# Performance work log

Measured on AMD Instinct MI355X. Metric: run time of the kernel, lower is better.

The kernel has to match this reference:

```python
import jax, jax.numpy as jnp
import numpy as np

HEADS = 8
DIM = 64
L = 2
P = 4  # hard-coded p_num in the torch module


def conv2d(x, w, b=None, pad=0, groups=1):
    y = jax.lax.conv_general_dilated(x, w, (1, 1), [(pad, pad), (pad, pad)],
        dimension_numbers=('NCHW', 'OIHW', 'NCHW'), feature_group_count=groups)
    return y if b is None else y + b[None, :, None, None]


def conv3d(x, w, pad=1, groups=1):
    return jax.lax.conv_general_dilated(x, w, (1, 1, 1), [(pad, pad)] * 3,
        dimension_numbers=('NCDHW', 'OIDHW', 'NCDHW'), feature_group_count=groups)


def pw(x, w):  # 1x1 conv, w: [O, C]
    return jnp.einsum('oc,bchw->bohw', w, x)


def layernorm(x, w, b):  # WithBias_LayerNorm over channel dim of NCHW
    mu = x.mean(axis=1, keepdims=True)
    var = ((x - mu) ** 2).mean(axis=1, keepdims=True)
    return (x - mu) / jnp.sqrt(var + 1e-5) * w[None, :, None, None] + b[None, :, None, None]


def l2n(x):  # F.normalize(dim=-1, p=2)
    return x / jnp.maximum(jnp.linalg.norm(x, axis=-1, keepdims=True), 1e-12)


def gelu(x):
    return jax.nn.gelu(x, approximate=False)


def spec_attn(x, mask, wq, wk, wv, dwq, dwk, dwv, resc, wp, mp1, mp2):
    b, c, h, w = x.shape
    ch = c // HEADS
    q = conv2d(pw(x, wq), dwq, pad=1, groups=c).reshape(b, HEADS, ch, h * w)
    k = conv2d(pw(x, wk), dwk, pad=1, groups=c).reshape(b, HEADS, ch, h * w)
    v = conv2d(pw(x, wv), dwv, pad=1, groups=c).reshape(b, HEADS, ch, h * w)
    q, k = l2n(q), l2n(k)
    att = jnp.einsum('bhcn,bhdn->bhcd', q, k) * resc[None, :, None, None]
    mb = pw(jax.nn.relu(conv2d(mask, mp1, pad=1)), mp2).mean(axis=(2, 3)).reshape(b, HEADS, ch)
    att = att + mb[:, :, None, :] - mb[:, :, :, None]
    att = jax.nn.softmax(att, axis=-1)
    out = jnp.einsum('bhcd,bhdn->bhcn', att, v).reshape(b, c, h, w)
    return pw(out, wp)


def ffn2d(x, w1, w2):  # PreNorm: dwconv3x3 (groups=dim, out=4*dim) -> GELU -> 1x1
    return pw(gelu(conv2d(x, w1, pad=1, groups=DIM)), w2)


def pol_attn(x, mask, wq, wk, wv, pwt, pb, resc, m1w, m1b, m2w, m2b):
    bp, c, h, w = x.shape
    bn = bp // P
    ch = c // HEADS
    xt = x.reshape(bn, P, c, h, w).transpose(0, 3, 4, 1, 2).reshape(bn * h * w, P, c)
    def heads_(t):
        return t.reshape(-1, P, HEADS, ch).transpose(0, 2, 1, 3)
    q = l2n(heads_(xt @ wq.T))
    k = l2n(heads_(xt @ wk.T))
    v = heads_(xt @ wv.T)
    att = jnp.einsum('bhpc,bhqc->bhpq', q, k) * resc[None, :, None, None]
    mg = pw(gelu(conv2d(mask, m1w, m1b, pad=1, groups=c)), m2w) + m2b[None, :, None, None]
    mg = mg.reshape(bn, P, c, h, w).mean(axis=2).transpose(0, 2, 3, 1).reshape(bn * h * w, P)
    att = att + (mg[:, None, :] - mg[:, :, None])[:, None]
    att = jax.nn.softmax(att, axis=-1)
    o = jnp.einsum('bhpq,bhqc->bhpc', att, v).transpose(0, 2, 1, 3).reshape(-1, P, c)
    o = o @ pwt.T + pb
    return o.reshape(bn, h, w, P, c).transpose(0, 3, 4, 1, 2).reshape(bp, c, h, w)


def ffn3d(x, w1, w2):  # PreNorm_Pols: 3D dwconv over (p,h,w) -> GELU -> 1x1x1
    bp, c, h, w = x.shape
    bn = bp // P
    y = x.reshape(bn, P, c, h, w).transpose(0, 2, 1, 3, 4)  # [bn, c, p, h, w]
    y = gelu(conv3d(y, w1, pad=1, groups=DIM))
    y = jnp.einsum('oc,bcdhw->bodhw', w2, y)
    return y.transpose(0, 2, 1, 3, 4).reshape(bp, c, h, w)


def forward(x, mask, sl1w, sl1b, sl2w, sl2b, swq, swk, swv, sdq, sdk, sdv, sresc, sproj,
            smp1, smp2, sf1, sf2, pl1w, pl1b, pl2w, pl2b, pwq, pwk, pwv, ppw, ppb, presc,
            pm1w, pm1b, pm2w, pm2b, pf1, pf2, fw1, fb1, fw2, fb2):
    # PSAM with type='pols': spectral branch + cross-polar branch + sigmoid fusion
    xs = x
    for i in range(L):
        xs = spec_attn(layernorm(xs, sl1w[i], sl1b[i]), mask, swq[i], swk[i], swv[i],
                       sdq[i], sdk[i], sdv[i], sresc[i], sproj[i], smp1[i], smp2[i]) + xs
        xs = ffn2d(layernorm(xs, sl2w[i], sl2b[i]), sf1[i], sf2[i]) + xs
    xp = x
    for i in range(L):
        xp = pol_attn(layernorm(xp, pl1w[i], pl1b[i]), mask, pwq[i], pwk[i], pwv[i],
                      ppw[i], ppb[i], presc[i], pm1w[i], pm1b[i], pm2w[i], pm2b[i]) + xp
        xp = ffn3d(layernorm(xp, pl2w[i], pl2b[i]), pf1[i], pf2[i]) + xp
    fu = jnp.concatenate([xs, xp], axis=1)
    a = jax.nn.sigmoid(conv2d(jax.nn.relu(pw(fu, fw1) + fb1[None, :, None, None]), fw2, fb2, pad=1))
    return a * xs + (1 - a) * xp


def setup_inputs():
    key = jax.random.key(0)
    D, H, Lb, B = DIM, HEADS, L, 8
    cnt = [0]
    def nrm(shape, s=0.02):
        cnt[0] += 1
        return jax.random.normal(jax.random.fold_in(key, cnt[0]), shape, jnp.float32) * s
    d = {}
    d['x'] = jax.random.normal(jax.random.fold_in(key, 1000), (B, D, 128, 128), jnp.float32)
    d['mask'] = jax.random.uniform(jax.random.fold_in(key, 1001), (B, D, 128, 128), jnp.float32)
    d['sl1w'] = jnp.ones((Lb, D)); d['sl1b'] = jnp.zeros((Lb, D))
    d['sl2w'] = jnp.ones((Lb, D)); d['sl2b'] = jnp.zeros((Lb, D))
    for n in ['swq', 'swk', 'swv', 'sproj', 'smp2']:
        d[n] = nrm((Lb, D, D))
    for n in ['sdq', 'sdk', 'sdv']:
        d[n] = nrm((Lb, D, 1, 3, 3))
    d['smp1'] = nrm((Lb, D, D, 3, 3))
    d['sresc'] = jnp.ones((Lb, H))
    d['sf1'] = nrm((Lb, 4 * D, 1, 3, 3)); d['sf2'] = nrm((Lb, D, 4 * D))
    d['pl1w'] = jnp.ones((Lb, D)); d['pl1b'] = jnp.zeros((Lb, D))
    d['pl2w'] = jnp.ones((Lb, D)); d['pl2b'] = jnp.zeros((Lb, D))
    for n in ['pwq', 'pwk', 'pwv', 'ppw', 'pm2w']:
        d[n] = nrm((Lb, D, D))
    d['ppb'] = jnp.zeros((Lb, D)); d['presc'] = jnp.ones((Lb, H))
    d['pm1w'] = nrm((Lb, D, 1, 3, 3)); d['pm1b'] = jnp.zeros((Lb, D)); d['pm2b'] = jnp.zeros((Lb, D))
    d['pf1'] = nrm((Lb, 4 * D, 1, 3, 3, 3)); d['pf2'] = nrm((Lb, D, 4 * D))
    d['fw1'] = nrm((D, 2 * D)); d['fb1'] = jnp.zeros((D,))
    d['fw2'] = nrm((D, D, 3, 3)); d['fb2'] = jnp.zeros((D,))
    return d


def reference(x, mask, sl1w, sl1b, sl2w, sl2b, swq, swk, swv, sdq, sdk, sdv, sresc, sproj,
              smp1, smp2, sf1, sf2, pl1w, pl1b, pl2w, pl2b, pwq, pwk, pwv, ppw, ppb, presc,
              pm1w, pm1b, pm2w, pm2b, pf1, pf2, fw1, fb1, fw2, fb2):
    return forward(x, mask, sl1w, sl1b, sl2w, sl2b, swq, swk, swv, sdq, sdk, sdv, sresc, sproj,
                   smp1, smp2, sf1, sf2, pl1w, pl1b, pl2w, pl2b, pwq, pwk, pwv, ppw, ppb, presc,
                   pm1w, pm1b, pm2w, pm2b, pf1, pf2, fw1, fb1, fw2, fb2)
```

## Files before the change

kernel.cpp:

```cpp
#include <hip/hip_runtime.h>
#include <math.h>

#define NPIX 16384
#define SBUF 8388608

__device__ __forceinline__ float gelu_f(float x){
    return 0.5f*x*(1.0f+erff(x*0.70710678118654752440f));
}
__device__ __forceinline__ float waveReduceSum(float v){
    #pragma unroll
    for(int off=32;off>0;off>>=1) v += __shfl_down(v, off);
    return v;
}

__global__ __launch_bounds__(256) void ln_kernel(const float* __restrict__ x,
        const float* __restrict__ w, const float* __restrict__ b, float* __restrict__ out){
    int idx = blockIdx.x*256 + threadIdx.x;
    int bb = idx >> 14, n = idx & 16383;
    const float* ip = x + ((size_t)bb<<20) + n;
    float v[64]; float s = 0.f;
    #pragma unroll
    for(int c=0;c<64;c++){ v[c] = ip[(size_t)c<<14]; s += v[c]; }
    float mu = s*(1.f/64.f); float ss = 0.f;
    #pragma unroll
    for(int c=0;c<64;c++){ float d = v[c]-mu; ss += d*d; }
    float r = rsqrtf(ss*(1.f/64.f) + 1e-5f);
    float* op = out + ((size_t)bb<<20) + n;
    #pragma unroll
    for(int c=0;c<64;c++) op[(size_t)c<<14] = (v[c]-mu)*r*w[c] + b[c];
}

__global__ __launch_bounds__(256) void pw_kernel(const float* __restrict__ in,
        const float* __restrict__ w, const float* __restrict__ bias,
        const float* __restrict__ res, float* __restrict__ out, int wPerB){
    __shared__ float wl[4096];
    int t = threadIdx.x;
    int idx = blockIdx.x*256 + t;
    int b = idx >> 14, n = idx & 16383;
    const float* wp = w + (wPerB ? b*4096 : 0);
    for(int i=t;i<4096;i+=256) wl[(i&63)*64 + (i>>6)] = wp[i];
    __syncthreads();
    float acc[64];
    if(bias){
        #pragma unroll
        for(int o=0;o<64;o++) acc[o] = bias[o];
    } else {
        #pragma unroll
        for(int o=0;o<64;o++) acc[o] = 0.f;
    }
    const float* ip = in + ((size_t)b<<20) + n;
    for(int c=0;c<64;c++){
        float v = ip[(size_t)c<<14];
        const float4* wv = (const float4*)&wl[c*64];
        #pragma unroll
        for(int o4=0;o4<16;o4++){
            float4 w4 = wv[o4];
            acc[o4*4+0] += w4.x*v; acc[o4*4+1] += w4.y*v;
            acc[o4*4+2] += w4.z*v; acc[o4*4+3] += w4.w*v;
        }
    }
    size_t baseo = ((size_t)b<<20) + n;
    if(res){
        #pragma unroll
        for(int o=0;o<64;o++) out[baseo+((size_t)o<<14)] = acc[o] + res[baseo+((size_t)o<<14)];
    } else {
        #pragma unroll
        for(int o=0;o<64;o++) out[baseo+((size_t)o<<14)] = acc[o];
    }
}

__global__ __launch_bounds__(256) void dw3x3_kernel(const float* __restrict__ in,
        const float* __restrict__ wd, float* __restrict__ out){
    int idx = blockIdx.x*256 + threadIdx.x;
    int n = idx & 16383; int bc = idx >> 14; int c = bc & 63;
    int y = n >> 7, x = n & 127;
    bool ym=y>0, yp=y<127, xm=x>0, xpv=x<127;
    const float* cp = in + ((size_t)bc<<14) + n;
    const float* wp = wd + c*9;
    float s = cp[0]*wp[4];
    if(ym){ s += cp[-128]*wp[1]; if(xm) s += cp[-129]*wp[0]; if(xpv) s += cp[-127]*wp[2]; }
    if(xm)  s += cp[-1]*wp[3];
    if(xpv) s += cp[1]*wp[5];
    if(yp){ s += cp[128]*wp[7]; if(xm) s += cp[127]*wp[6]; if(xpv) s += cp[129]*wp[8]; }
    out[idx] = s;
}

__global__ __launch_bounds__(256) void l2n_kernel(float* __restrict__ q){
    int bc = blockIdx.x;
    float* p = q + ((size_t)bc<<14);
    int t = threadIdx.x;
    float ss = 0.f;
    for(int n=t;n<NPIX;n+=256){ float v=p[n]; ss += v*v; }
    ss = waveReduceSum(ss);
    __shared__ float red[4];
    __shared__ float scale_s;
    if((t&63)==0) red[t>>6] = ss;
    __syncthreads();
    if(t==0) scale_s = 1.f/fmaxf(sqrtf(red[0]+red[1]+red[2]+red[3]), 1e-12f);
    __syncthreads();
    float sc = scale_s;
    for(int n=t;n<NPIX;n+=256) p[n] *= sc;
}

__global__ __launch_bounds__(256) void qk_kernel(const float* __restrict__ Q,
        const float* __restrict__ K, float* __restrict__ att){
    int blk = blockIdx.x;
    int c = blk & 7, bh = blk >> 3;
    const float* qp = Q + (((size_t)bh*8 + c)<<14);
    const float* kp = K + (((size_t)bh*8)<<14);
    float p[8] = {0,0,0,0,0,0,0,0};
    for(int n=threadIdx.x;n<NPIX;n+=256){
        float qv = qp[n];
        #pragma unroll
        for(int d=0;d<8;d++) p[d] += qv*kp[((size_t)d<<14)+n];
    }
    #pragma unroll
    for(int off=32;off>0;off>>=1){
        #pragma unroll
        for(int d=0;d<8;d++) p[d] += __shfl_down(p[d], off);
    }
    __shared__ float red[4][8];
    int wave = threadIdx.x>>6, lane = threadIdx.x&63;
    if(lane==0){
        #pragma unroll
        for(int d=0;d<8;d++) red[wave][d] = p[d];
    }
    __syncthreads();
    if(threadIdx.x<8){
        float s = red[0][threadIdx.x]+red[1][threadIdx.x]+red[2][threadIdx.x]+red[3][threadIdx.x];
        att[blk*8+threadIdx.x] = s;
    }
}

__global__ void zero512(float* __restrict__ p){
    p[blockIdx.x*256 + threadIdx.x] = 0.f;
}

__global__ __launch_bounds__(256) void mbconv4_kernel(const float* __restrict__ mask,
        const float* __restrict__ w, float* __restrict__ svec){
    __shared__ float wl[9216];
    __shared__ float red[4][16];
    int t = threadIdx.x;
    int og = blockIdx.x & 3;
    int pb = (blockIdx.x >> 2) & 31;
    int b  = blockIdx.x >> 7;
    const float* wp = w + (size_t)og*16*576;
    for(int i=t;i<9216;i+=256){
        int mo = i & 15, ck = i >> 4;
        wl[i] = wp[mo*576 + ck];
    }
    __syncthreads();
    int n0 = pb*512 + t;
    int n1 = n0 + 256;
    int y0 = n0>>7, x0 = n0&127;
    int y1 = n1>>7, x1 = n1&127;
    bool ym0=y0>0, yp0=y0<127, xm0=x0>0, xp0=x0<127;
    bool ym1=y1>0, yp1=y1<127, xm1=x1>0, xp1=x1<127;
    const float* mp = mask + ((size_t)b<<20);
    float acc0[16], acc1[16];
    #pragma unroll
    for(int o=0;o<16;o++){ acc0[o]=0.f; acc1[o]=0.f; }
    for(int c=0;c<64;c++){
        const float* cp0 = mp + ((size_t)c<<14) + n0;
        const float* cp1 = mp + ((size_t)c<<14) + n1;
        float ta[9], tb[9];
        ta[0] = (ym0&&xm0)? cp0[-129]:0.f;
        ta[1] =  ym0?       cp0[-128]:0.f;
        ta[2] = (ym0&&xp0)? cp0[-127]:0.f;
        ta[3] =  xm0?       cp0[-1]:0.f;
        ta[4] =             cp0[0];
        ta[5] =  xp0?       cp0[1]:0.f;
        ta[6] = (yp0&&xm0)? cp0[127]:0.f;
        ta[7] =  yp0?       cp0[128]:0.f;
        ta[8] = (yp0&&xp0)? cp0[129]:0.f;
        tb[0] = (ym1&&xm1)? cp1[-129]:0.f;
        tb[1] =  ym1?       cp1[-128]:0.f;
        tb[2] = (ym1&&xp1)? cp1[-127]:0.f;
        tb[3] =  xm1?       cp1[-1]:0.f;
        tb[4] =             cp1[0];
        tb[5] =  xp1?       cp1[1]:0.f;
        tb[6] = (yp1&&xm1)? cp1[127]:0.f;
        tb[7] =  yp1?       cp1[128]:0.f;
        tb[8] = (yp1&&xp1)? cp1[129]:0.f;
        #pragma unroll
        for(int k=0;k<9;k++){
            float va = ta[k], vb = tb[k];
            const float4* wv = (const float4*)&wl[(c*9+k)*16];
            #pragma unroll
            for(int o4=0;o4<4;o4++){
                float4 w4 = wv[o4];
                acc0[o4*4+0] += w4.x*va; acc0[o4*4+1] += w4.y*va;
                acc0[o4*4+2] += w4.z*va; acc0[o4*4+3] += w4.w*va;
                acc1[o4*4+0] += w4.x*vb; acc1[o4*4+1] += w4.y*vb;
                acc1[o4*4+2] += w4.z*vb; acc1[o4*4+3] += w4.w*vb;
            }
        }
    }
    int wave = t>>6, lane = t&63;
    #pragma unroll
    for(int m=0;m<16;m++){
        float v = waveReduceSum(fmaxf(acc0[m],0.f) + fmaxf(acc1[m],0.f));
        if(lane==0) red[wave][m] = v;
    }
    __syncthreads();
    if(t<16){
        float s = red[0][t]+red[1][t]+red[2][t]+red[3][t];
        atomicAdd(&svec[b*64 + og*16 + t], s);
    }
}

__global__ void spec_softmax_kernel(float* __restrict__ att, const float* __restrict__ svec,
        const float* __restrict__ smp2, const float* __restrict__ resc){
    int b = blockIdx.x, t = threadIdx.x;
    __shared__ float mb[64];
    float a = 0.f;
    for(int m=0;m<64;m++) a += smp2[t*64+m]*svec[b*64+m];
    mb[t] = a*(1.f/16384.f);
    __syncthreads();
    int h = t>>3, c = t&7;
    float* ap = att + (size_t)(b*8+h)*64 + c*8;
    float rs = resc[h];
    float v[8]; float mx = -1e30f;
    #pragma unroll
    for(int d=0;d<8;d++){ v[d] = ap[d]*rs + mb[h*8+d] - mb[h*8+c]; mx = fmaxf(mx, v[d]); }
    float s = 0.f;
    #pragma unroll
    for(int d=0;d<8;d++){ v[d] = expf(v[d]-mx); s += v[d]; }
    float inv = 1.f/s;
    #pragma unroll
    for(int d=0;d<8;d++) ap[d] = v[d]*inv;
}

__global__ void mmat_kernel(const float* __restrict__ att, const float* __restrict__ sproj,
        float* __restrict__ M){
    int b = blockIdx.x;
    for(int e=threadIdx.x;e<4096;e+=256){
        int o = e>>6, j = e&63;
        int h = j>>3, jj = j&7;
        float s = 0.f;
        #pragma unroll
        for(int cc=0;cc<8;cc++) s += sproj[o*64 + h*8+cc]*att[(size_t)(b*8+h)*64 + cc*8 + jj];
        M[b*4096 + e] = s;
    }
}

__global__ __launch_bounds__(256) void ffn2d_kernel(const float* __restrict__ A,
        const float* __restrict__ w1, const float* __restrict__ w2, float* __restrict__ xs){
    __shared__ float w2l[16384];
    int t = threadIdx.x;
    for(int i=t;i<16384;i+=256){ int o=i>>8, m=i&255; w2l[m*64+o] = w2[i]; }
    __syncthreads();
    int idx = blockIdx.x*256 + t;
    int b = idx>>14, n = idx&16383;
    int y = n>>7, x = n&127;
    bool ym=y>0, yp=y<127, xm=x>0, xpv=x<127;
    const float* ap = A + ((size_t)b<<20) + n;
    float acc[64];
    #pragma unroll
    for(int o=0;o<64;o++) acc[o] = 0.f;
    for(int c=0;c<64;c++){
        const float* cp = ap + ((size_t)c<<14);
        float t00 = (ym&&xm)? cp[-129]:0.f;
        float t01 =  ym?      cp[-128]:0.f;
        float t02 = (ym&&xpv)?cp[-127]:0.f;
        float t10 =  xm?      cp[-1]:0.f;
        float t11 =           cp[0];
        float t12 =  xpv?     cp[1]:0.f;
        float t20 = (yp&&xm)? cp[127]:0.f;
        float t21 =  yp?      cp[128]:0.f;
        float t22 = (yp&&xpv)?cp[129]:0.f;
        const float* w1c = w1 + c*36;
        #pragma unroll
        for(int j=0;j<4;j++){
            const float* wj = w1c + j*9;
            float cv = t00*wj[0]+t01*wj[1]+t02*wj[2]+t10*wj[3]+t11*wj[4]
                      +t12*wj[5]+t20*wj[6]+t21*wj[7]+t22*wj[8];
            float g = gelu_f(cv);
            const float4* wv = (const float4*)&w2l[(c*4+j)*64];
            #pragma unroll
            for(int o4=0;o4<16;o4++){
                float4 w4 = wv[o4];
                acc[o4*4+0] += w4.x*g; acc[o4*4+1] += w4.y*g;
                acc[o4*4+2] += w4.z*g; acc[o4*4+3] += w4.w*g;
            }
        }
    }
    size_t baseo = ((size_t)b<<20) + n;
    #pragma unroll
    for(int o=0;o<64;o++) xs[baseo+((size_t)o<<14)] += acc[o];
}

__global__ void wbar_kernel(const float* __restrict__ pm2w, const float* __restrict__ pm2b,
        float* __restrict__ wbar){
    int t = threadIdx.x;
    float s = 0.f;
    for(int o=0;o<64;o++) s += pm2w[o*64+t];
    wbar[t] = s*(1.f/64.f);
    if(t==0){
        float sb = 0.f;
        for(int o=0;o<64;o++) sb += pm2b[o];
        wbar[64] = sb*(1.f/64.f);
    }
}

__global__ __launch_bounds__(256) void mg_kernel(const float* __restrict__ mask,
        const float* __restrict__ w1, const float* __restrict__ b1,
        const float* __restrict__ wbar, float* __restrict__ mg){
    int idx = blockIdx.x*256 + threadIdx.x;
    int b = idx>>14, n = idx&16383;
    int y = n>>7, x = n&127;
    bool ym=y>0, yp=y<127, xm=x>0, xpv=x<127;
    const float* ap = mask + ((size_t)b<<20) + n;
    float acc = wbar[64];
    for(int c=0;c<64;c++){
        const float* cp = ap + ((size_t)c<<14);
        const float* wj = w1 + c*9;
        float cv = b1[c] + cp[0]*wj[4];
        if(ym){ cv += cp[-128]*wj[1]; if(xm) cv += cp[-129]*wj[0]; if(xpv) cv += cp[-127]*wj[2]; }
        if(xm)  cv += cp[-1]*wj[3];
        if(xpv) cv += cp[1]*wj[5];
        if(yp){ cv += cp[128]*wj[7]; if(xm) cv += cp[127]*wj[6]; if(xpv) cv += cp[129]*wj[8]; }
        acc += wbar[c]*gelu_f(cv);
    }
    mg[idx] = acc;
}

__global__ __launch_bounds__(256) void att_pol_kernel(const float* __restrict__ Q,
        const float* __restrict__ K, const float* __restrict__ V,
        const float* __restrict__ mg, const float* __restrict__ resc, float* __restrict__ O){
    int idx = blockIdx.x*256 + threadIdx.x;
    int bn = idx>>14, n = idx&16383;
    float mgv[4];
    #pragma unroll
    for(int p=0;p<4;p++) mgv[p] = mg[(((bn<<2)+p)<<14) + n];
    for(int h=0;h<8;h++){
        size_t base = ((size_t)bn<<22) + ((size_t)h<<17) + n;
        float q[4][8], k[4][8], v[4][8];
        #pragma unroll
        for(int p=0;p<4;p++){
            size_t pb = base + ((size_t)p<<20);
            #pragma unroll
            for(int j=0;j<8;j++){
                size_t o = pb + ((size_t)j<<14);
                q[p][j] = Q[o]; k[p][j] = K[o]; v[p][j] = V[o];
            }
        }
        #pragma unroll
        for(int p=0;p<4;p++){
            float sq=0.f, sk=0.f;
            #pragma unroll
            for(int j=0;j<8;j++){ sq += q[p][j]*q[p][j]; sk += k[p][j]*k[p][j]; }
            float iq = 1.f/fmaxf(sqrtf(sq),1e-12f), ik = 1.f/fmaxf(sqrtf(sk),1e-12f);
            #pragma unroll
            for(int j=0;j<8;j++){ q[p][j]*=iq; k[p][j]*=ik; }
        }
        float rs = resc[h];
        float att[4][4];
        #pragma unroll
        for(int p=0;p<4;p++){
            #pragma unroll
            for(int r=0;r<4;r++){
                float d = 0.f;
                #pragma unroll
                for(int j=0;j<8;j++) d += q[p][j]*k[r][j];
                att[p][r] = rs*d + mgv[r] - mgv[p];
            }
        }
        #pragma unroll
        for(int p=0;p<4;p++){
            float mx = fmaxf(fmaxf(att[p][0],att[p][1]),fmaxf(att[p][2],att[p][3]));
            float s = 0.f;
            #pragma unroll
            for(int r=0;r<4;r++){ att[p][r] = expf(att[p][r]-mx); s += att[p][r]; }
            float inv = 1.f/s;
            #pragma unroll
            for(int r=0;r<4;r++) att[p][r] *= inv;
        }
        #pragma unroll
        for(int p=0;p<4;p++){
            size_t pb = base + ((size_t)p<<20);
            #pragma unroll
            for(int j=0;j<8;j++){
                float o = att[p][0]*v[0][j]+att[p][1]*v[1][j]+att[p][2]*v[2][j]+att[p][3]*v[3][j];
                O[pb + ((size_t)j<<14)] = o;
            }
        }
    }
}

__global__ __launch_bounds__(256) void ffn3d_kernel(const float* __restrict__ A,
        const float* __restrict__ w1, const float* __restrict__ w2, float* __restrict__ xp){
    __shared__ float w2l[16384];
    int t = threadIdx.x;
    for(int i=t;i<16384;i+=256){ int o=i>>8, m=i&255; w2l[m*64+o] = w2[i]; }
    __syncthreads();
    int idx = blockIdx.x*256 + t;
    int bp = idx>>14, n = idx&16383;
    int bn = bp>>2, p = bp&3;
    int y = n>>7, x = n&127;
    bool ym=y>0, yp=y<127, xm=x>0, xpv=x<127;
    float acc[64];
    #pragma unroll
    for(int o=0;o<64;o++) acc[o] = 0.f;
    for(int c=0;c<64;c++){
        float tap[27];
        #pragma unroll
        for(int dz=0;dz<3;dz++){
            int pp = p + dz - 1;
            if(pp < 0 || pp > 3){
                #pragma unroll
                for(int k9=0;k9<9;k9++) tap[dz*9+k9] = 0.f;
            } else {
                const float* cp = A + ((size_t)((bn<<2)+pp)<<20) + ((size_t)c<<14) + n;
                tap[dz*9+0] = (ym&&xm)? cp[-129]:0.f;
                tap[dz*9+1] =  ym?      cp[-128]:0.f;
                tap[dz*9+2] = (ym&&xpv)?cp[-127]:0.f;
                tap[dz*9+3] =  xm?      cp[-1]:0.f;
                tap[dz*9+4] =           cp[0];
                tap[dz*9+5] =  xpv?     cp[1]:0.f;
                tap[dz*9+6] = (yp&&xm)? cp[127]:0.f;
                tap[dz*9+7] =  yp?      cp[128]:0.f;
                tap[dz*9+8] = (yp&&xpv)?cp[129]:0.f;
            }
        }
        const float* w1c = w1 + c*108;
        #pragma unroll
        for(int j=0;j<4;j++){
            const float* wj = w1c + j*27;
            float cv = 0.f;
            #pragma unroll
            for(int k27=0;k27<27;k27++) cv += tap[k27]*wj[k27];
            float g = gelu_f(cv);
            const float4* wv = (const float4*)&w2l[(c*4+j)*64];
            #pragma unroll
            for(int o4=0;o4<16;o4++){
                float4 w4 = wv[o4];
                acc[o4*4+0] += w4.x*g; acc[o4*4+1] += w4.y*g;
                acc[o4*4+2] += w4.z*g; acc[o4*4+3] += w4.w*g;
            }
        }
    }
    size_t baseo = ((size_t)bp<<20) + n;
    #pragma unroll
    for(int o=0;o<64;o++) xp[baseo+((size_t)o<<14)] += acc[o];
}

__global__ __launch_bounds__(256) void fuse1_kernel(const float* __restrict__ xs,
        const float* __restrict__ xp, const float* __restrict__ fw1,
        const float* __restrict__ fb1, float* __restrict__ T){
    __shared__ float wl[8192];
    int t = threadIdx.x;
    for(int i=t;i<8192;i+=256) wl[(i&127)*64 + (i>>7)] = fw1[i];
    __syncthreads();
    int idx = blockIdx.x*256 + t;
    int b = idx>>14, n = idx&16383;
    float acc[64];
    #pragma unroll
    for(int o=0;o<64;o++) acc[o] = fb1[o];
    const float* ip = xs + ((size_t)b<<20) + n;
    for(int c=0;c<64;c++){
        float v = ip[(size_t)c<<14];
        const float4* wv = (const float4*)&wl[c*64];
        #pragma unroll
        for(int o4=0;o4<16;o4++){
            float4 w4 = wv[o4];
            acc[o4*4+0] += w4.x*v; acc[o4*4+1] += w4.y*v;
            acc[o4*4+2] += w4.z*v; acc[o4*4+3] += w4.w*v;
        }
    }
    const float* ip2 = xp + ((size_t)b<<20) + n;
    for(int c=0;c<64;c++){
        float v = ip2[(size_t)c<<14];
        const float4* wv = (const float4*)&wl[(64+c)*64];
        #pragma unroll
        for(int o4=0;o4<16;o4++){
            float4 w4 = wv[o4];
            acc[o4*4+0] += w4.x*v; acc[o4*4+1] += w4.y*v;
            acc[o4*4+2] += w4.z*v; acc[o4*4+3] += w4.w*v;
        }
    }
    size_t baseo = ((size_t)b<<20) + n;
    #pragma unroll
    for(int o=0;o<64;o++) T[baseo+((size_t)o<<14)] = fmaxf(acc[o], 0.f);
}

__global__ __launch_bounds__(256) void fuse2v2_kernel(const float* __restrict__ T,
        const float* __restrict__ fw2, const float* __restrict__ fb2,
        const float* __restrict__ xs, const float* __restrict__ xp, float* __restrict__ out){
    __shared__ float wl[9216];
    int t = threadIdx.x;
    int og = blockIdx.x & 3;
    int pb = (blockIdx.x >> 2) & 31;
    int b  = blockIdx.x >> 7;
    const float* wp = fw2 + (size_t)og*16*576;
    for(int i=t;i<9216;i+=256){
        int mo = i & 15, ck = i >> 4;
        wl[i] = wp[mo*576 + ck];
    }
    __syncthreads();
    int n0 = pb*512 + t;
    int n1 = n0 + 256;
    int y0 = n0>>7, x0 = n0&127;
    int y1 = n1>>7, x1 = n1&127;
    bool ym0=y0>0, yp0=y0<127, xm0=x0>0, xp0=x0<127;
    bool ym1=y1>0, yp1=y1<127, xm1=x1>0, xp1=x1<127;
    const float* tp = T + ((size_t)b<<20);
    float acc0[16], acc1[16];
    #pragma unroll
    for(int o=0;o<16;o++){ acc0[o]=0.f; acc1[o]=0.f; }
    for(int c=0;c<64;c++){
        const float* cp0 = tp + ((size_t)c<<14) + n0;
        const float* cp1 = tp + ((size_t)c<<14) + n1;
        float ta[9], tb[9];
        ta[0] = (ym0&&xm0)? cp0[-129]:0.f;
        ta[1] =  ym0?       cp0[-128]:0.f;
        ta[2] = (ym0&&xp0)? cp0[-127]:0.f;
        ta[3] =  xm0?       cp0[-1]:0.f;
        ta[4] =             cp0[0];
        ta[5] =  xp0?       cp0[1]:0.f;
        ta[6] = (yp0&&xm0)? cp0[127]:0.f;
        ta[7] =  yp0?       cp0[128]:0.f;
        ta[8] = (yp0&&xp0)? cp0[129]:0.f;
        tb[0] = (ym1&&xm1)? cp1[-129]:0.f;
        tb[1] =  ym1?       cp1[-128]:0.f;
        tb[2] = (ym1&&xp1)? cp1[-127]:0.f;
        tb[3] =  xm1?       cp1[-1]:0.f;
        tb[4] =             cp1[0];
        tb[5] =  xp1?       cp1[1]:0.f;
        tb[6] = (yp1&&xm1)? cp1[127]:0.f;
        tb[7] =  yp1?       cp1[128]:0.f;
        tb[8] = (yp1&&xp1)? cp1[129]:0.f;
        #pragma unroll
        for(int k=0;k<9;k++){
            float va = ta[k], vb = tb[k];
            const float4* wv = (const float4*)&wl[(c*9+k)*16];
            #pragma unroll
            for(int o4=0;o4<4;o4++){
                float4 w4 = wv[o4];
                acc0[o4*4+0] += w4.x*va; acc0[o4*4+1] += w4.y*va;
                acc0[o4*4+2] += w4.z*va; acc0[o4*4+3] += w4.w*va;
                acc1[o4*4+0] += w4.x*vb; acc1[o4*4+1] += w4.y*vb;
                acc1[o4*4+2] += w4.z*vb; acc1[o4*4+3] += w4.w*vb;
            }
        }
    }
    #pragma unroll
    for(int m=0;m<16;m++){
        int o = og*16 + m;
        float bias = fb2[o];
        size_t i0 = ((size_t)b<<20) + ((size_t)o<<14) + n0;
        size_t i1 = ((size_t)b<<20) + ((size_t)o<<14) + n1;
        float a0 = 1.f/(1.f+expf(-(acc0[m]+bias)));
        float a1 = 1.f/(1.f+expf(-(acc1[m]+bias)));
        out[i0] = a0*xs[i0] + (1.f-a0)*xp[i0];
        out[i1] = a1*xs[i1] + (1.f-a1)*xp[i1];
    }
}

extern "C" void kernel_launch(void* const* d_in, const int* in_sizes, int n_in,
                              void* d_out, int out_size, void* d_ws, size_t ws_size,
                              hipStream_t stream) {
    const float* x     = (const float*)d_in[0];
    const float* mask  = (const float*)d_in[1];
    const float* sl1w  = (const float*)d_in[2];
    const float* sl1b  = (const float*)d_in[3];
    const float* sl2w  = (const float*)d_in[4];
    const float* sl2b  = (const float*)d_in[5];
    const float* swq   = (const float*)d_in[6];
    const float* swk   = (const float*)d_in[7];
    const float* swv   = (const float*)d_in[8];
    const float* sproj = (const float*)d_in[9];
    const float* smp2  = (const float*)d_in[10];
    const float* sdq   = (const float*)d_in[11];
    const float* sdk   = (const float*)d_in[12];
    const float* sdv   = (const float*)d_in[13];
    const float* smp1  = (const float*)d_in[14];
    const float* sresc = (const float*)d_in[15];
    const float* sf1   = (const float*)d_in[16];
    const float* sf2   = (const float*)d_in[17];
    const float* pl1w  = (const float*)d_in[18];
    const float* pl1b  = (const float*)d_in[19];
    const float* pl2w  = (const float*)d_in[20];
    const float* pl2b  = (const float*)d_in[21];
    const float* pwq   = (const float*)d_in[22];
    const float* pwk   = (const float*)d_in[23];
    const float* pwv   = (const float*)d_in[24];
    const float* ppw   = (const float*)d_in[25];
    const float* pm2w  = (const float*)d_in[26];
    const float* ppb   = (const float*)d_in[27];
    const float* presc = (const float*)d_in[28];
    const float* pm1w  = (const float*)d_in[29];
    const float* pm1b  = (const float*)d_in[30];
    const float* pm2b  = (const float*)d_in[31];
    const float* pf1   = (const float*)d_in[32];
    const float* pf2   = (const float*)d_in[33];
    const float* fw1   = (const float*)d_in[34];
    const float* fb1   = (const float*)d_in[35];
    const float* fw2   = (const float*)d_in[36];
    const float* fb2   = (const float*)d_in[37];

    float* ws_f = (float*)d_ws;
    float* xs = ws_f;
    float* xp = ws_f + (size_t)SBUF;
    float* A  = ws_f + 2*(size_t)SBUF;
    float* Q  = ws_f + 3*(size_t)SBUF;
    float* K  = ws_f + 4*(size_t)SBUF;
    float* V  = ws_f + 5*(size_t)SBUF;
    float* small = ws_f + 6*(size_t)SBUF;
    float* mg   = small;
    float* att  = mg + 131072;
    float* svec = att + 4096;
    float* M    = svec + 512;
    float* wbar = M + 32768;
    float* stage = (float*)d_out;
    float* Tf = Q;

    hipMemcpyAsync(xs, x, (size_t)SBUF*4, hipMemcpyDeviceToDevice, stream);
    hipMemcpyAsync(xp, x, (size_t)SBUF*4, hipMemcpyDeviceToDevice, stream);

    for(int i=0;i<2;i++){
        ln_kernel<<<512,256,0,stream>>>(xs, sl1w+i*64, sl1b+i*64, A);
        pw_kernel<<<512,256,0,stream>>>(A, swq+i*4096, nullptr, nullptr, stage, 0);
        dw3x3_kernel<<<32768,256,0,stream>>>(stage, sdq+i*576, Q);
        pw_kernel<<<512,256,0,stream>>>(A, swk+i*4096, nullptr, nullptr, stage, 0);
        dw3x3_kernel<<<32768,256,0,stream>>>(stage, sdk+i*576, K);
        pw_kernel<<<512,256,0,stream>>>(A, swv+i*4096, nullptr, nullptr, stage, 0);
        dw3x3_kernel<<<32768,256,0,stream>>>(stage, sdv+i*576, V);
        l2n_kernel<<<512,256,0,stream>>>(Q);
        l2n_kernel<<<512,256,0,stream>>>(K);
        qk_kernel<<<512,256,0,stream>>>(Q, K, att);
        zero512<<<2,256,0,stream>>>(svec);
        mbconv4_kernel<<<1024,256,0,stream>>>(mask, smp1+i*36864, svec);
        spec_softmax_kernel<<<8,64,0,stream>>>(att, svec, smp2+i*4096, sresc+i*8);
        mmat_kernel<<<8,256,0,stream>>>(att, sproj+i*4096, M);
        pw_kernel<<<512,256,0,stream>>>(V, M, nullptr, xs, xs, 1);
        ln_kernel<<<512,256,0,stream>>>(xs, sl2w+i*64, sl2b+i*64, A);
        ffn2d_kernel<<<512,256,0,stream>>>(A, sf1+i*2304, sf2+i*16384, xs);
    }
    for(int i=0;i<2;i++){
        ln_kernel<<<512,256,0,stream>>>(xp, pl1w+i*64, pl1b+i*64, A);
        pw_kernel<<<512,256,0,stream>>>(A, pwq+i*4096, nullptr, nullptr, Q, 0);
        pw_kernel<<<512,256,0,stream>>>(A, pwk+i*4096, nullptr, nullptr, K, 0);
        pw_kernel<<<512,256,0,stream>>>(A, pwv+i*4096, nullptr, nullptr, V, 0);
        wbar_kernel<<<1,64,0,stream>>>(pm2w+i*4096, pm2b+i*64, wbar);
        mg_kernel<<<512,256,0,stream>>>(mask, pm1w+i*576, pm1b+i*64, wbar, mg);
        att_pol_kernel<<<128,256,0,stream>>>(Q, K, V, mg, presc+i*8, stage);
        pw_kernel<<<512,256,0,stream>>>(stage, ppw+i*4096, ppb+i*64, xp, xp, 0);
        ln_kernel<<<512,256,0,stream>>>(xp, pl2w+i*64, pl2b+i*64, A);
        ffn3d_kernel<<<512,256,0,stream>>>(A, pf1+i*6912, pf2+i*16384, xp);
    }
    fuse1_kernel<<<512,256,0,stream>>>(xs, xp, fw1, fb1, Tf);
    fuse2v2_kernel<<<1024,256,0,stream>>>(Tf, fw2, fb2, xs, xp, (float*)d_out);
}
```

Measured before the change: 3.199 ms.

## Split FFN output channels across four blocks to raise parallelism and occupancy

```diff
diff --git a/kernel.cpp b/kernel.cpp
--- a/kernel.cpp
+++ b/kernel.cpp
@@ -244,20 +244,25 @@
     }
 }
 
-__global__ __launch_bounds__(256) void ffn2d_kernel(const float* __restrict__ A,
+__global__ __launch_bounds__(256) void ffn2d_v3_kernel(const float* __restrict__ A,
         const float* __restrict__ w1, const float* __restrict__ w2, float* __restrict__ xs){
-    __shared__ float w2l[16384];
-    int t = threadIdx.x;
-    for(int i=t;i<16384;i+=256){ int o=i>>8, m=i&255; w2l[m*64+o] = w2[i]; }
-    __syncthreads();
-    int idx = blockIdx.x*256 + t;
-    int b = idx>>14, n = idx&16383;
+    __shared__ float w2l[4096];
+    int t = threadIdx.x;
+    int og = blockIdx.x & 3;
+    int pb = (blockIdx.x >> 2) & 63;
+    int b  = blockIdx.x >> 8;
+    for(int i=t;i<4096;i+=256){
+        int oo = i & 15, m = i >> 4;
+        w2l[i] = w2[(og*16+oo)*256 + m];
+    }
+    __syncthreads();
+    int n = pb*256 + t;
     int y = n>>7, x = n&127;
     bool ym=y>0, yp=y<127, xm=x>0, xpv=x<127;
     const float* ap = A + ((size_t)b<<20) + n;
-    float acc[64];
-    #pragma unroll
-    for(int o=0;o<64;o++) acc[o] = 0.f;
+    float acc[16];
+    #pragma unroll
+    for(int o=0;o<16;o++) acc[o] = 0.f;
     for(int c=0;c<64;c++){
         const float* cp = ap + ((size_t)c<<14);
         float t00 = (ym&&xm)? cp[-129]:0.f;
@@ -276,18 +281,18 @@
             float cv = t00*wj[0]+t01*wj[1]+t02*wj[2]+t10*wj[3]+t11*wj[4]
                       +t12*wj[5]+t20*wj[6]+t21*wj[7]+t22*wj[8];
             float g = gelu_f(cv);
-            const float4* wv = (const float4*)&w2l[(c*4+j)*64];
-            #pragma unroll
-            for(int o4=0;o4<16;o4++){
+            const float4* wv = (const float4*)&w2l[(c*4+j)*16];
+            #pragma unroll
+            for(int o4=0;o4<4;o4++){
                 float4 w4 = wv[o4];
                 acc[o4*4+0] += w4.x*g; acc[o4*4+1] += w4.y*g;
                 acc[o4*4+2] += w4.z*g; acc[o4*4+3] += w4.w*g;
             }
         }
     }
-    size_t baseo = ((size_t)b<<20) + n;
-    #pragma unroll
-    for(int o=0;o<64;o++) xs[baseo+((size_t)o<<14)] += acc[o];
+    size_t baseo = ((size_t)b<<20) + ((size_t)(og*16)<<14) + n;
+    #pragma unroll
+    for(int o=0;o<16;o++) xs[baseo+((size_t)o<<14)] += acc[o];
 }
 
 __global__ void wbar_kernel(const float* __restrict__ pm2w, const float* __restrict__ pm2b,
@@ -388,20 +393,25 @@
     }
 }
 
-__global__ __launch_bounds__(256) void ffn3d_kernel(const float* __restrict__ A,
+__global__ __launch_bounds__(256) void ffn3d_v3_kernel(const float* __restrict__ A,
         const float* __restrict__ w1, const float* __restrict__ w2, float* __restrict__ xp){
-    __shared__ float w2l[16384];
-    int t = threadIdx.x;
-    for(int i=t;i<16384;i+=256){ int o=i>>8, m=i&255; w2l[m*64+o] = w2[i]; }
-    __syncthreads();
-    int idx = blockIdx.x*256 + t;
-    int bp = idx>>14, n = idx&16383;
+    __shared__ float w2l[4096];
+    int t = threadIdx.x;
+    int og = blockIdx.x & 3;
+    int pbk = (blockIdx.x >> 2) & 63;
+    int bp = blockIdx.x >> 8;
+    for(int i=t;i<4096;i+=256){
+        int oo = i & 15, m = i >> 4;
+        w2l[i] = w2[(og*16+oo)*256 + m];
+    }
+    __syncthreads();
     int bn = bp>>2, p = bp&3;
+    int n = pbk*256 + t;
     int y = n>>7, x = n&127;
     bool ym=y>0, yp=y<127, xm=x>0, xpv=x<127;
-    float acc[64];
-    #pragma unroll
-    for(int o=0;o<64;o++) acc[o] = 0.f;
+    float acc[16];
+    #pragma unroll
+    for(int o=0;o<16;o++) acc[o] = 0.f;
     for(int c=0;c<64;c++){
         float tap[27];
         #pragma unroll
@@ -431,18 +441,18 @@
             #pragma unroll
             for(int k27=0;k27<27;k27++) cv += tap[k27]*wj[k27];
             float g = gelu_f(cv);
-            const float4* wv = (const float4*)&w2l[(c*4+j)*64];
-            #pragma unroll
-            for(int o4=0;o4<16;o4++){
+            const float4* wv = (const float4*)&w2l[(c*4+j)*16];
+            #pragma unroll
+            for(int o4=0;o4<4;o4++){
                 float4 w4 = wv[o4];
                 acc[o4*4+0] += w4.x*g; acc[o4*4+1] += w4.y*g;
                 acc[o4*4+2] += w4.z*g; acc[o4*4+3] += w4.w*g;
             }
         }
     }
-    size_t baseo = ((size_t)bp<<20) + n;
-    #pragma unroll
-    for(int o=0;o<64;o++) xp[baseo+((size_t)o<<14)] += acc[o];
+    size_t baseo = ((size_t)bp<<20) + ((size_t)(og*16)<<14) + n;
+    #pragma unroll
+    for(int o=0;o<16;o++) xp[baseo+((size_t)o<<14)] += acc[o];
 }
 
 __global__ __launch_bounds__(256) void fuse1_kernel(const float* __restrict__ xs,
@@ -635,7 +645,7 @@
         mmat_kernel<<<8,256,0,stream>>>(att, sproj+i*4096, M);
         pw_kernel<<<512,256,0,stream>>>(V, M, nullptr, xs, xs, 1);
         ln_kernel<<<512,256,0,stream>>>(xs, sl2w+i*64, sl2b+i*64, A);
-        ffn2d_kernel<<<512,256,0,stream>>>(A, sf1+i*2304, sf2+i*16384, xs);
+        ffn2d_v3_kernel<<<2048,256,0,stream>>>(A, sf1+i*2304, sf2+i*16384, xs);
     }
     for(int i=0;i<2;i++){
         ln_kernel<<<512,256,0,stream>>>(xp, pl1w+i*64, pl1b+i*64, A);
@@ -647,7 +657,7 @@
         att_pol_kernel<<<128,256,0,stream>>>(Q, K, V, mg, presc+i*8, stage);
         pw_kernel<<<512,256,0,stream>>>(stage, ppw+i*4096, ppb+i*64, xp, xp, 0);
         ln_kernel<<<512,256,0,stream>>>(xp, pl2w+i*64, pl2b+i*64, A);
-        ffn3d_kernel<<<512,256,0,stream>>>(A, pf1+i*6912, pf2+i*16384, xp);
+        ffn3d_v3_kernel<<<2048,256,0,stream>>>(A, pf1+i*6912, pf2+i*16384, xp);
     }
     fuse1_kernel<<<512,256,0,stream>>>(xs, xp, fw1, fb1, Tf);
     fuse2v2_kernel<<<1024,256,0,stream>>>(Tf, fw2, fb2, xs, xp, (float*)d_out);
```

Result: faster. 2.933 ms (-8.3%).
